# Performance work log

Hardware: AMD Instinct MI355X
Metric: run time of the kernel (lower is better)

The kernel has to match this reference:

```python
import jax, jax.numpy as jnp
import numpy as np

# hardcoded constants from the source module
C = 768      # n_embd
H = 8        # n_head
HS = C // H  # head_size = 96
E = 8        # n_experts
K = 2        # top_k
L = 12       # n_layer
V = 95       # vocab_size = len(chars)
BS = 64      # block_size
B, T = 16, 64


def setup_inputs() -> dict:
    key = jax.random.key(0)
    ks = iter(jax.random.split(key, 32))
    nrm = lambda shape: jax.random.normal(next(ks), shape, dtype=jnp.float32) * 0.02
    d = {
        'idx': jax.random.randint(next(ks), (B, T), 0, V),
        'tok_emb': nrm((V, C)),
        'pos_emb': nrm((BS, C)),
        # attention (per-layer stacked); per-head q/k/v linears concatenated into [C, C]
        'Wq': nrm((L, C, C)), 'Wk': nrm((L, C, C)), 'Wv': nrm((L, C, C)),
        'Wo': nrm((L, C, C)), 'bo': jnp.zeros((L, C), jnp.float32),
        # MoE
        'gate_W': nrm((L, C, E)), 'gate_b': jnp.zeros((L, E), jnp.float32),
        'W1': nrm((L, E, C, 4 * C)), 'b1': jnp.zeros((L, E, 4 * C), jnp.float32),
        'W2': nrm((L, E, 4 * C, C)), 'b2': jnp.zeros((L, E, C), jnp.float32),
        # layernorms
        'ln1_g': jnp.ones((L, C), jnp.float32), 'ln1_b': jnp.zeros((L, C), jnp.float32),
        'ln2_g': jnp.ones((L, C), jnp.float32), 'ln2_b': jnp.zeros((L, C), jnp.float32),
        'lnf_g': jnp.ones((C,), jnp.float32), 'lnf_b': jnp.zeros((C,), jnp.float32),
        # lm head
        'head_W': nrm((C, V)), 'head_b': jnp.zeros((V,), jnp.float32),
    }
    return d


def _layernorm(x, g, b, eps=1e-5):
    mu = x.mean(-1, keepdims=True)
    var = ((x - mu) ** 2).mean(-1, keepdims=True)
    return (x - mu) * jax.lax.rsqrt(var + eps) * g + b


def _moe(x, gw, gb, w1, b1, w2, b2):
    # x: [B,T,C]; compute all experts densely then combine top-k (faithful to source)
    xf = x.reshape(-1, C)                                  # [N,C]
    probs = jax.nn.softmax(xf @ gw + gb, axis=-1)          # [N,E]
    tp, ti = jax.lax.top_k(probs, K)                       # [N,K]
    tp = tp / tp.sum(-1, keepdims=True)
    h = jax.nn.gelu(jnp.einsum('nc,ech->neh', xf, w1) + b1, approximate=False)
    eo = jnp.einsum('neh,ehc->nec', h, w2) + b2            # [N,E,C]
    sel = jnp.take_along_axis(eo, ti[:, :, None], axis=1)  # [N,K,C]
    return (tp[:, :, None] * sel).sum(1).reshape(x.shape)


def _forward(idx, tok_emb, pos_emb, Wq, Wk, Wv, Wo, bo, gate_W, gate_b, W1, b1,
             W2, b2, ln1_g, ln1_b, ln2_g, ln2_b, lnf_g, lnf_b, head_W, head_b):
    Bc, Tc = idx.shape
    x = tok_emb[idx] + pos_emb[jnp.arange(Tc) % BS]        # [B,T,C]
    mask = jnp.tril(jnp.ones((Tc, Tc), bool))

    def block(x, p):
        q = (x @ p['Wq']).reshape(Bc, Tc, H, HS)
        k = (x @ p['Wk']).reshape(Bc, Tc, H, HS)
        v = (x @ p['Wv']).reshape(Bc, Tc, H, HS)
        att = jnp.einsum('bqhd,bkhd->bhqk', q, k) * (HS ** -0.5)
        att = jnp.where(mask, att, -jnp.inf)
        w = jax.nn.softmax(att, axis=-1)
        o = jnp.einsum('bhqk,bkhd->bqhd', w, v).reshape(Bc, Tc, C)
        y = o @ p['Wo'] + p['bo']
        x = _layernorm(x + y, p['g1'], p['b1n'])
        y = _moe(x, p['gw'], p['gb'], p['w1'], p['bb1'], p['w2'], p['bb2'])
        x = _layernorm(x + y, p['g2'], p['b2n'])
        return x, None

    params = {'Wq': Wq, 'Wk': Wk, 'Wv': Wv, 'Wo': Wo, 'bo': bo,
              'gw': gate_W, 'gb': gate_b, 'w1': W1, 'bb1': b1, 'w2': W2, 'bb2': b2,
              'g1': ln1_g, 'b1n': ln1_b, 'g2': ln2_g, 'b2n': ln2_b}
    x, _ = jax.lax.scan(block, x, params)
    x = _layernorm(x, lnf_g, lnf_b)
    return x @ head_W + head_b                              # [B,T,V]


def reference(idx, tok_emb, pos_emb, Wq, Wk, Wv, Wo, bo, gate_W, gate_b, W1, b1,
              W2, b2, ln1_g, ln1_b, ln2_g, ln2_b, lnf_g, lnf_b, head_W, head_b):
    return _forward(idx, tok_emb, pos_emb, Wq, Wk, Wv, Wo, bo, gate_W, gate_b,
                    W1, b1, W2, b2, ln1_g, ln1_b, ln2_g, ln2_b, lnf_g, lnf_b,
                    head_W, head_b)
```

## Files before the change

kernel.cpp:

```cpp
#include <hip/hip_runtime.h>
#include <math.h>

#define C    768
#define HN   8
#define HS   96
#define NE   8
#define NL   12
#define NV   95
#define TT   64
#define NB   16
#define NTOK 1024
#define H4   3072
#define NKR  2048
#define NKRP 2176
#define MC   (NTOK * C)

typedef __attribute__((ext_vector_type(8))) short short8;
typedef __attribute__((ext_vector_type(4))) float floatx4;

union U16x8 { uint4 u; short8 s; };
static __device__ __forceinline__ short8 as_s8(uint4 u) { U16x8 x; x.u = u; return x.s; }
static __device__ __forceinline__ uint4 ror16x4(uint4 q) {
  uint4 r;
  r.x = (q.x >> 16) | (q.x << 16);
  r.y = (q.y >> 16) | (q.y << 16);
  r.z = (q.z >> 16) | (q.z << 16);
  r.w = (q.w >> 16) | (q.w << 16);
  return r;
}

static __device__ __forceinline__ unsigned pack_split(float f) {
  unsigned u = __float_as_uint(f);
  unsigned h = (u + 0x7fffu + ((u >> 16) & 1u)) >> 16;
  float d = f - __uint_as_float(h << 16);
  unsigned v = __float_as_uint(d);
  unsigned l = (v + 0x7fffu + ((v >> 16) & 1u)) >> 16;
  return h | (l << 16);
}
static __device__ __forceinline__ float unpack_split(unsigned w) {
  return __uint_as_float(w << 16) + __uint_as_float(w & 0xffff0000u);
}

static __device__ __forceinline__ void gload_lds16(const unsigned* g, unsigned* l) {
  __builtin_amdgcn_global_load_lds(
      (const __attribute__((address_space(1))) unsigned*)g,
      (__attribute__((address_space(3))) unsigned*)l, 16, 0, 0);
}

__global__ void __launch_bounds__(256) k_prep(const float* __restrict__ src,
    unsigned* __restrict__ dst, int K, int N, long matStride, long dstMatStride) {
  int nt = blockIdx.x, kt = blockIdx.y, mz = blockIdx.z;
  const float* W = src + (size_t)mz * matStride;
  unsigned* out = dst + (size_t)mz * dstMatStride
                + ((size_t)nt * (K >> 5) + kt) * 4096;
  __shared__ float ls[32 * 130];
  int tid = threadIdx.x;
  int n0 = nt * 128, k0 = kt * 32;
  #pragma unroll
  for (int p = 0; p < 16; ++p) {
    int idx = p * 256 + tid;
    int k = idx >> 7, c = idx & 127;
    int n = n0 + c;
    ls[k * 130 + c] = (n < N) ? W[(size_t)(k0 + k) * N + n] : 0.f;
  }
  __syncthreads();
  #pragma unroll
  for (int p = 0; p < 16; ++p) {
    int idx = p * 256 + tid;
    int col = idx >> 5, ks = idx & 31;
    int k = ks ^ ((col & 7) << 2);
    out[idx] = pack_split(ls[k * 130 + col]);
  }
}

template<int OUTMODE>
static __device__ __forceinline__ void gemm_body(
    const unsigned* __restrict__ Ap, const int* __restrict__ perm,
    const unsigned* __restrict__ Wt, const float* __restrict__ bias,
    float* __restrict__ outF, unsigned* __restrict__ outP,
    int row0, int Mend, int col0, int N, int K, int kbeg, int kend)
{
  __shared__ __align__(16) unsigned Bt[2][64 * 32];
  const int tid  = threadIdx.x;
  const int lane = tid & 63, wv = tid >> 6;
  const int l16  = lane & 15, lq = lane >> 4;
  const int sw   = (l16 & 7) << 2;

  int ra0 = row0 + wv * 32 + l16;
  int ra1 = ra0 + 16;
  if (ra0 > Mend - 1) ra0 = Mend - 1;
  if (ra1 > Mend - 1) ra1 = Mend - 1;
  if (perm) { ra0 = perm[ra0]; ra1 = perm[ra1]; }
  const unsigned* A0 = Ap + (size_t)ra0 * K;
  const unsigned* A1 = Ap + (size_t)ra1 * K;

  const unsigned* tsrc = Wt + ((size_t)(col0 >> 7) * (K >> 5) + (kbeg >> 5)) * 4096
                       + ((size_t)((col0 >> 6) & 1)) * 2048;
  auto stageB = [&](int buf, int kt) {
    const unsigned* s = tsrc + (size_t)kt * 4096 + wv * 512 + lane * 4;
    unsigned* d = &Bt[buf][wv * 512 + lane * 4];
    gload_lds16(s, d);
    gload_lds16(s + 256, d + 256);
  };

  uint4 ac0[2], ac1[2];
  auto loadA = [&](int kpos, uint4* d0, uint4* d1) {
    const unsigned* p = A0 + kpos;
    d0[0] = *(const uint4*)(p + lq * 4);
    d0[1] = *(const uint4*)(p + 16 + lq * 4);
    p = A1 + kpos;
    d1[0] = *(const uint4*)(p + lq * 4);
    d1[1] = *(const uint4*)(p + 16 + lq * 4);
  };

  floatx4 acc[2][4];
  #pragma unroll
  for (int h = 0; h < 2; ++h)
    #pragma unroll
    for (int f = 0; f < 4; ++f) acc[h][f] = (floatx4){0, 0, 0, 0};

  const int ns = (kend - kbeg) >> 5;
  stageB(0, 0);
  loadA(kbeg, ac0, ac1);

  for (int s = 0; s < ns; ++s) {
    const int b = s & 1;
    __syncthreads();
    if (s + 1 < ns) stageB(b ^ 1, s + 1);
    const int kn = kbeg + ((s + 1 < ns) ? (s + 1) * 32 : s * 32);
    uint4 na0[2], na1[2];
    loadA(kn, na0, na1);
    const unsigned* bp = Bt[b];
    #pragma unroll
    for (int f = 0; f < 4; ++f) {
      const unsigned* base = bp + (f * 16 + l16) * 32;
      uint4 q0 = *(const uint4*)(base + ((4 * lq) ^ sw));
      uint4 q1 = *(const uint4*)(base + ((16 + 4 * lq) ^ sw));
      short8 b0 = as_s8(q0), b0r = as_s8(ror16x4(q0));
      short8 b1 = as_s8(q1), b1r = as_s8(ror16x4(q1));
      short8 a00 = as_s8(ac0[0]), a01 = as_s8(ac0[1]);
      short8 a10 = as_s8(ac1[0]), a11 = as_s8(ac1[1]);
      acc[0][f] = __builtin_amdgcn_mfma_f32_16x16x32_bf16(a00, b0,  acc[0][f], 0, 0, 0);
      acc[1][f] = __builtin_amdgcn_mfma_f32_16x16x32_bf16(a10, b0,  acc[1][f], 0, 0, 0);
      acc[0][f] = __builtin_amdgcn_mfma_f32_16x16x32_bf16(a00, b0r, acc[0][f], 0, 0, 0);
      acc[1][f] = __builtin_amdgcn_mfma_f32_16x16x32_bf16(a10, b0r, acc[1][f], 0, 0, 0);
      acc[0][f] = __builtin_amdgcn_mfma_f32_16x16x32_bf16(a01, b1,  acc[0][f], 0, 0, 0);
      acc[1][f] = __builtin_amdgcn_mfma_f32_16x16x32_bf16(a11, b1,  acc[1][f], 0, 0, 0);
      acc[0][f] = __builtin_amdgcn_mfma_f32_16x16x32_bf16(a01, b1r, acc[0][f], 0, 0, 0);
      acc[1][f] = __builtin_amdgcn_mfma_f32_16x16x32_bf16(a11, b1r, acc[1][f], 0, 0, 0);
    }
    ac0[0] = na0[0]; ac0[1] = na0[1]; ac1[0] = na1[0]; ac1[1] = na1[1];
  }

  const int rb = row0 + wv * 32 + lq * 4;
  #pragma unroll
  for (int h = 0; h < 2; ++h) {
    #pragma unroll
    for (int f = 0; f < 4; ++f) {
      int cc = col0 + f * 16 + l16;
      if (cc < N) {
        float bb = (OUTMODE == 1) ? bias[cc] : 0.f;
        #pragma unroll
        for (int r = 0; r < 4; ++r) {
          int rr = rb + h * 16 + r;
          if (rr < Mend) {
            float v = acc[h][f][r] + bb;
            if (OUTMODE == 1) {
              v = 0.5f * v * (1.f + erff(v * 0.70710678118654752f));
              outP[(size_t)rr * N + cc] = pack_split(v);
            } else {
              outF[(size_t)rr * N + cc] = v;
            }
          }
        }
      }
    }
  }
}

static __device__ __forceinline__ void expert_range(const int* counts, int e,
                                                    int& off, int& cnt) {
  off = 0; cnt = 0;
  #pragma unroll
  for (int i = 0; i < NE; ++i) {
    int c = counts[i];
    if (i < e) off += c;
    if (i == e) cnt = c;
  }
}

__global__ void __launch_bounds__(256, 2) k_qkv(const unsigned* xp, const unsigned* Wq,
    const unsigned* Wk, const unsigned* Wv, float* qkvp) {
  int z = blockIdx.z, mat = z >> 1, ch = z & 1;
  const unsigned* W = mat == 0 ? Wq : (mat == 1 ? Wk : Wv);
  gemm_body<2>(xp, nullptr, W, nullptr, qkvp + (size_t)z * MC, nullptr,
               blockIdx.y * 128, NTOK, blockIdx.x * 64, C, C, ch * 384, (ch + 1) * 384);
}

__global__ void __launch_bounds__(256, 2) k_wo(const unsigned* op, const unsigned* W,
    float* wop) {
  int ch = blockIdx.z;
  gemm_body<2>(op, nullptr, W, nullptr, wop + (size_t)ch * MC, nullptr,
               blockIdx.y * 128, NTOK, blockIdx.x * 64, C, C, ch * 128, (ch + 1) * 128);
}

__global__ void __launch_bounds__(256, 2) k_w1(const unsigned* xp, const int* perm,
    const unsigned* W1, const float* b1, unsigned* Hgp, const int* counts) {
  int e = blockIdx.z, off, cnt;
  expert_range(counts, e, off, cnt);
  int r0 = blockIdx.y * 128;
  if (r0 >= cnt) return;
  gemm_body<1>(xp, perm, W1 + (size_t)e * C * H4, b1 + (size_t)e * H4, nullptr, Hgp,
               off + r0, off + cnt, blockIdx.x * 64, H4, C, 0, C);
}

__global__ void __launch_bounds__(256, 2) k_w2(const unsigned* Hgp, const unsigned* W2,
    float* Ypart, const int* counts) {
  int z = blockIdx.z, e = z >> 2, ch = z & 3;
  int off, cnt;
  expert_range(counts, e, off, cnt);
  int r0 = blockIdx.y * 128;
  if (r0 >= cnt) return;
  gemm_body<2>(Hgp, nullptr, W2 + (size_t)e * H4 * C, nullptr,
               Ypart + (size_t)ch * NKRP * C, nullptr,
               off + r0, off + cnt, blockIdx.x * 64, C, H4, ch * 768, (ch + 1) * 768);
}

__global__ void __launch_bounds__(256, 2) k_head(const unsigned* xp, const unsigned* W,
    float* hpart) {
  int ch = blockIdx.z;
  gemm_body<2>(xp, nullptr, W, nullptr, hpart + (size_t)ch * NTOK * NV, nullptr,
               blockIdx.y * 128, NTOK, blockIdx.x * 64, NV, C, ch * 64, (ch + 1) * 64);
}

__global__ void k_headsum(const float* hpart, const float* headb, float* out) {
  int n = blockIdx.x, c = threadIdx.x;
  if (c < NV) {
    size_t i = (size_t)n * NV + c;
    float s = headb[c];
    #pragma unroll
    for (int ch = 0; ch < 12; ++ch) s += hpart[i + (size_t)ch * NTOK * NV];
    out[i] = s;
  }
}

__global__ void k_embed(const int* __restrict__ idx, const float* __restrict__ tok,
                        const float* __restrict__ pos, unsigned* __restrict__ xp) {
  int n = blockIdx.x; int t = n & (TT - 1);
  int token = idx[n];
  for (int j = threadIdx.x; j < C; j += 256)
    xp[(size_t)n * C + j] = pack_split(tok[(size_t)token * C + j] + pos[(size_t)t * C + j]);
}

static __device__ __forceinline__ void ln_finish(int tid, float* v, const float* g,
                                                 const float* bb, unsigned* outrow,
                                                 float* sp) {
  int lane = tid & 63, wid = tid >> 6;
  float s = v[0] + v[1] + v[2];
  for (int o = 32; o; o >>= 1) s += __shfl_down(s, o);
  if (!lane) sp[wid] = s;
  __syncthreads();
  float mean = (sp[0] + sp[1] + sp[2] + sp[3]) * (1.f / C);
  __syncthreads();
  float d0 = v[0] - mean, d1 = v[1] - mean, d2 = v[2] - mean;
  float qq = d0 * d0 + d1 * d1 + d2 * d2;
  for (int o = 32; o; o >>= 1) qq += __shfl_down(qq, o);
  if (!lane) sp[wid] = qq;
  __syncthreads();
  float var = (sp[0] + sp[1] + sp[2] + sp[3]) * (1.f / C);
  float rs = rsqrtf(var + 1e-5f);
  #pragma unroll
  for (int i = 0; i < 3; ++i) {
    int c = tid + i * 256;
    v[i] = (v[i] - mean) * rs * g[c] + bb[c];
    outrow[c] = pack_split(v[i]);
  }
}

__global__ void __launch_bounds__(256) k_ln1g(unsigned* __restrict__ xp,
    const float* __restrict__ wop, const float* __restrict__ bo,
    const float* __restrict__ g, const float* __restrict__ bb,
    const float* __restrict__ gW, const float* __restrict__ gb,
    int* __restrict__ ti, float* __restrict__ tp, int* __restrict__ pos,
    int* __restrict__ counts) {
  int n = blockIdx.x; int tid = threadIdx.x;
  __shared__ float sp[4];
  __shared__ float gs[4][NE];
  float v[3];
  #pragma unroll
  for (int i = 0; i < 3; ++i) {
    int c = tid + i * 256;
    size_t gi = (size_t)n * C + c;
    float acc = unpack_split(xp[gi]) + bo[c];
    #pragma unroll
    for (int ch = 0; ch < 6; ++ch) acc += wop[gi + (size_t)ch * MC];
    v[i] = acc;
  }
  ln_finish(tid, v, g, bb, xp + (size_t)n * C, sp);
  float a[NE];
  #pragma unroll
  for (int e = 0; e < NE; ++e) a[e] = 0.f;
  #pragma unroll
  for (int i = 0; i < 3; ++i) {
    int c = tid + i * 256;
    const float* gr = gW + (size_t)c * NE;
    #pragma unroll
    for (int e = 0; e < NE; ++e) a[e] += v[i] * gr[e];
  }
  int lane = tid & 63, wid = tid >> 6;
  #pragma unroll
  for (int e = 0; e < NE; ++e)
    for (int o = 32; o; o >>= 1) a[e] += __shfl_down(a[e], o);
  if (!lane)
    #pragma unroll
    for (int e = 0; e < NE; ++e) gs[wid][e] = a[e];
  __syncthreads();
  if (tid == 0) {
    float p[NE]; float m = -1e30f;
    #pragma unroll
    for (int e = 0; e < NE; ++e) {
      p[e] = gs[0][e] + gs[1][e] + gs[2][e] + gs[3][e] + gb[e];
      m = fmaxf(m, p[e]);
    }
    float den = 0.f;
    #pragma unroll
    for (int e = 0; e < NE; ++e) { p[e] = expf(p[e] - m); den += p[e]; }
    float inv = 1.f / den;
    #pragma unroll
    for (int e = 0; e < NE; ++e) p[e] *= inv;
    int e0 = 0;
    for (int e = 1; e < NE; ++e) if (p[e] > p[e0]) e0 = e;
    int e1 = -1;
    for (int e = 0; e < NE; ++e) if (e != e0 && (e1 < 0 || p[e] > p[e1])) e1 = e;
    float ss = p[e0] + p[e1];
    int p0 = atomicAdd(&counts[e0], 1), p1 = atomicAdd(&counts[e1], 1);
    ti[n * 2] = e0;  ti[n * 2 + 1] = e1;
    pos[n * 2] = p0; pos[n * 2 + 1] = p1;
    tp[n * 2] = p[e0] / ss; tp[n * 2 + 1] = p[e1] / ss;
  }
}

__global__ void k_perm(const int* __restrict__ ti, const int* __restrict__ pos,
                       const int* __restrict__ counts, int* __restrict__ rowOf,
                       int* __restrict__ perm) {
  int a = blockIdx.x * 256 + threadIdx.x;
  if (a >= NKRP) return;
  if (a >= NKR) { perm[a] = 0; return; }
  int e = ti[a];
  int off = 0;
  #pragma unroll
  for (int i = 0; i < NE; ++i) if (i < e) off += counts[i];
  int row = off + pos[a];
  rowOf[a] = row;
  perm[row] = a >> 1;
}

__global__ void __launch_bounds__(256) k_ln_moe(unsigned* __restrict__ xp,
    const float* __restrict__ Ypart, const int* __restrict__ rowOf,
    const int* __restrict__ ti, const float* __restrict__ tp,
    const float* __restrict__ b2, const float* __restrict__ g,
    const float* __restrict__ bb) {
  int n = blockIdx.x; int tid = threadIdx.x;
  __shared__ float sp[4];
  int r0 = rowOf[n * 2], r1 = rowOf[n * 2 + 1];
  int e0 = ti[n * 2], e1 = ti[n * 2 + 1];
  float w0 = tp[n * 2], w1 = tp[n * 2 + 1];
  const float* bz0 = b2 + (size_t)e0 * C;
  const float* bz1 = b2 + (size_t)e1 * C;
  float v[3];
  #pragma unroll
  for (int i = 0; i < 3; ++i) {
    int c = tid + i * 256;
    float y0 = bz0[c], y1 = bz1[c];
    #pragma unroll
    for (int ch = 0; ch < 4; ++ch) {
      const float* pl = Ypart + (size_t)ch * NKRP * C;
      y0 += pl[(size_t)r0 * C + c];
      y1 += pl[(size_t)r1 * C + c];
    }
    v[i] = unpack_split(xp[(size_t)n * C + c]) + w0 * y0 + w1 * y1;
  }
  ln_finish(tid, v, g, bb, xp + (size_t)n * C, sp);
}

__global__ void __launch_bounds__(256) k_lnf(unsigned* __restrict__ xp,
    const float* __restrict__ g, const float* __restrict__ bb) {
  int n = blockIdx.x; int tid = threadIdx.x;
  __shared__ float sp[4];
  float v[3];
  #pragma unroll
  for (int i = 0; i < 3; ++i) v[i] = unpack_split(xp[(size_t)n * C + tid + i * 256]);
  ln_finish(tid, v, g, bb, xp + (size_t)n * C, sp);
}

__global__ void __launch_bounds__(256) k_attn(const float* __restrict__ qkvp,
    unsigned* __restrict__ op, int* __restrict__ counts) {
  int bh = blockIdx.x; int b = bh >> 3, h = bh & 7;
  int tid = threadIdx.x;
  if (bh == 0 && tid < NE) counts[tid] = 0;
  __shared__ float qs[TT][HS];
  __shared__ float kv[TT][HS];
  const float* q0 = qkvp;                  const float* q1 = qkvp + MC;
  const float* k0 = qkvp + 2 * (size_t)MC; const float* k1 = qkvp + 3 * (size_t)MC;
  const float* v0 = qkvp + 4 * (size_t)MC; const float* v1 = qkvp + 5 * (size_t)MC;
  for (int i = tid; i < TT * HS; i += 256) {
    int t = i / HS, d = i % HS;
    size_t gi = (size_t)(b * TT + t) * C + h * HS + d;
    qs[t][d] = q0[gi] + q1[gi];
    kv[t][d] = k0[gi] + k1[gi];
  }
  __syncthreads();
  int r = tid >> 2, g = tid & 3;
  const float scale = 0.10206207261596575f;
  float sreg[16];
  {
    const floatx4* q4 = (const floatx4*)&qs[r][0];
    #pragma unroll
    for (int j = 0; j < 16; ++j) {
      int kk = g * 16 + j;
      float s = -1e30f;
      if (kk <= r) {
        const floatx4* k4 = (const floatx4*)&kv[kk][0];
        float a2 = 0.f;
        #pragma unroll
        for (int d4 = 0; d4 < HS / 4; ++d4) {
          floatx4 a = q4[d4], bbv = k4[d4];
          a2 += a[0]*bbv[0] + a[1]*bbv[1] + a[2]*bbv[2] + a[3]*bbv[3];
        }
        s = a2 * scale;
      }
      sreg[j] = s;
    }
  }
  float m = sreg[0];
  #pragma unroll
  for (int j = 1; j < 16; ++j) m = fmaxf(m, sreg[j]);
  m = fmaxf(m, __shfl_xor(m, 1));
  m = fmaxf(m, __shfl_xor(m, 2));
  float den = 0.f;
  #pragma unroll
  for (int j = 0; j < 16; ++j) { sreg[j] = expf(sreg[j] - m); den += sreg[j]; }
  den += __shfl_xor(den, 1);
  den += __shfl_xor(den, 2);
  float inv = 1.f / den;
  __syncthreads();
  float (*psc)[TT] = (float(*)[TT])&qs[0][0];
  #pragma unroll
  for (int j = 0; j < 16; ++j) psc[r][g * 16 + j] = sreg[j] * inv;
  for (int i = tid; i < TT * HS; i += 256) {
    int t = i / HS, d = i % HS;
    size_t gi = (size_t)(b * TT + t) * C + h * HS + d;
    kv[t][d] = v0[gi] + v1[gi];
  }
  __syncthreads();
  floatx4 accv[6];
  #pragma unroll
  for (int cc = 0; cc < 6; ++cc) accv[cc] = (floatx4){0, 0, 0, 0};
  for (int kk = 0; kk < TT; ++kk) {
    float wgt = psc[r][kk];
    const floatx4* v4 = (const floatx4*)&kv[kk][0];
    #pragma unroll
    for (int cc = 0; cc < 6; ++cc) accv[cc] += wgt * v4[g * 6 + cc];
  }
  unsigned* orow = op + (size_t)(b * TT + r) * C + h * HS + g * 24;
  #pragma unroll
  for (int cc = 0; cc < 6; ++cc)
    #pragma unroll
    for (int mm = 0; mm < 4; ++mm) orow[cc * 4 + mm] = pack_split(accv[cc][mm]);
}

extern "C" void kernel_launch(void* const* d_in, const int* in_sizes, int n_in,
                              void* d_out, int out_size, void* d_ws, size_t ws_size,
                              hipStream_t stream) {
  const int*   idx   = (const int*)d_in[0];
  const float* tok   = (const float*)d_in[1];
  const float* pose  = (const float*)d_in[2];
  const float* Wq    = (const float*)d_in[3];
  const float* Wk    = (const float*)d_in[4];
  const float* Wv    = (const float*)d_in[5];
  const float* Wo    = (const float*)d_in[6];
  const float* bo    = (const float*)d_in[7];
  const float* gW    = (const float*)d_in[8];
  const float* gb    = (const float*)d_in[9];
  const float* W1    = (const float*)d_in[10];
  const float* b1    = (const float*)d_in[11];
  const float* W2    = (const float*)d_in[12];
  const float* b2    = (const float*)d_in[13];
  const float* ln1g  = (const float*)d_in[14];
  const float* ln1b  = (const float*)d_in[15];
  const float* ln2g  = (const float*)d_in[16];
  const float* ln2b  = (const float*)d_in[17];
  const float* lnfg  = (const float*)d_in[18];
  const float* lnfb  = (const float*)d_in[19];
  const float* headW = (const float*)d_in[20];
  const float* headb = (const float*)d_in[21];
  float* out = (float*)d_out;

  if (ws_size < (size_t)2200 * 1024 * 1024) return;
  char* w = (char*)d_ws;
  auto allocU = [&](size_t n) { unsigned* p = (unsigned*)w; w += n * 4; return p; };
  auto allocF = [&](size_t n) { float* p = (float*)w; w += n * 4; return p; };
  unsigned* Wqp = allocU((size_t)NL * C * C);
  unsigned* Wkp = allocU((size_t)NL * C * C);
  unsigned* Wvp = allocU((size_t)NL * C * C);
  unsigned* Wop = allocU((size_t)NL * C * C);
  unsigned* W1p = allocU((size_t)NL * NE * C * H4);
  unsigned* W2p = allocU((size_t)NL * NE * H4 * C);
  unsigned* Whp = allocU((size_t)24 * 4096);
  unsigned* xp    = allocU((size_t)MC);
  unsigned* op    = allocU((size_t)MC);
  float*    qkvp  = allocF((size_t)6 * MC);
  float*    wop   = allocF((size_t)6 * MC);
  unsigned* Hgp   = allocU((size_t)NKRP * H4);
  float*    Ypart = allocF((size_t)4 * NKRP * C);
  float*    hpart = allocF((size_t)12 * NTOK * NV);
  float*    tp    = allocF(NKR);
  int* ti     = (int*)w; w += NKR * 4;
  int* posA   = (int*)w; w += NKR * 4;
  int* rowOf  = (int*)w; w += NKR * 4;
  int* perm   = (int*)w; w += NKRP * 4;
  int* counts = (int*)w; w += NE * 4;

  k_prep<<<dim3(6, 24, 12), 256, 0, stream>>>(Wq, Wqp, C, C, (long)C * C, (long)C * C);
  k_prep<<<dim3(6, 24, 12), 256, 0, stream>>>(Wk, Wkp, C, C, (long)C * C, (long)C * C);
  k_prep<<<dim3(6, 24, 12), 256, 0, stream>>>(Wv, Wvp, C, C, (long)C * C, (long)C * C);
  k_prep<<<dim3(6, 24, 12), 256, 0, stream>>>(Wo, Wop, C, C, (long)C * C, (long)C * C);
  k_prep<<<dim3(24, 24, 96), 256, 0, stream>>>(W1, W1p, C, H4, (long)C * H4, (long)C * H4);
  k_prep<<<dim3(6, 96, 96), 256, 0, stream>>>(W2, W2p, H4, C, (long)H4 * C, (long)H4 * C);
  k_prep<<<dim3(1, 24, 1), 256, 0, stream>>>(headW, Whp, C, NV, 0, 0);

  k_embed<<<NTOK, 256, 0, stream>>>(idx, tok, pose, xp);

  for (int l = 0; l < NL; ++l) {
    k_qkv<<<dim3(12, 8, 6), 256, 0, stream>>>(
        xp, Wqp + (size_t)l * C * C, Wkp + (size_t)l * C * C, Wvp + (size_t)l * C * C, qkvp);
    k_attn<<<NB * HN, 256, 0, stream>>>(qkvp, op, counts);
    k_wo<<<dim3(12, 8, 6), 256, 0, stream>>>(op, Wop + (size_t)l * C * C, wop);
    k_ln1g<<<NTOK, 256, 0, stream>>>(xp, wop, bo + (size_t)l * C,
        ln1g + (size_t)l * C, ln1b + (size_t)l * C,
        gW + (size_t)l * C * NE, gb + (size_t)l * NE, ti, tp, posA, counts);
    k_perm<<<(NKRP + 255) / 256, 256, 0, stream>>>(ti, posA, counts, rowOf, perm);
    k_w1<<<dim3(48, 8, 8), 256, 0, stream>>>(xp, perm,
        W1p + (size_t)l * NE * C * H4, b1 + (size_t)l * NE * H4, Hgp, counts);
    k_w2<<<dim3(12, 8, 32), 256, 0, stream>>>(Hgp,
        W2p + (size_t)l * NE * H4 * C, Ypart, counts);
    k_ln_moe<<<NTOK, 256, 0, stream>>>(xp, Ypart, rowOf, ti, tp,
        b2 + (size_t)l * NE * C, ln2g + (size_t)l * C, ln2b + (size_t)l * C);
  }

  k_lnf<<<NTOK, 256, 0, stream>>>(xp, lnfg, lnfb);
  k_head<<<dim3(2, 8, 12), 256, 0, stream>>>(xp, Whp, hpart);
  k_headsum<<<NTOK, 128, 0, stream>>>(hpart, headb, out);
}
```

Before: 4.105 ms.

## Fuse all per-layer kernels into one persistent kernel with grid barriers

Replaces the dozens of per-layer kernel launches with a single persistent kernel of 512 blocks. Each block loops over the tiles of every stage and stages are separated by a software grid barrier built on a global atomic counter. Split-K factors for Wo and the head are also reduced from 6 and 12 chunks to 2, which shrinks the partial buffers and the reduction work. The aim is to remove launch overhead and inter-kernel gaps, at the cost of spin-barrier latency. The design assumes all 512 blocks are co-resident, and the grid can deadlock if they are not.

New measurement: 12.21 ms. 198% more time.

```diff
diff --git a/kernel.cpp b/kernel.cpp
--- a/kernel.cpp
+++ b/kernel.cpp
@@ -14,6 +14,7 @@
 #define NKR  2048
 #define NKRP 2176
 #define MC   (NTOK * C)
+#define NBLK 512
 
 typedef __attribute__((ext_vector_type(8))) short short8;
 typedef __attribute__((ext_vector_type(4))) float floatx4;
@@ -73,14 +74,24 @@
   }
 }
 
+__global__ void k_embed(const int* __restrict__ idx, const float* __restrict__ tok,
+                        const float* __restrict__ pos, unsigned* __restrict__ xp) {
+  int n = blockIdx.x; int t = n & (TT - 1);
+  int token = idx[n];
+  for (int j = threadIdx.x; j < C; j += 256)
+    xp[(size_t)n * C + j] = pack_split(tok[(size_t)token * C + j] + pos[(size_t)t * C + j]);
+}
+
 template<int OUTMODE>
-static __device__ __forceinline__ void gemm_body(
+static __device__ __forceinline__ void gemm_tile(
+    unsigned* shb,
     const unsigned* __restrict__ Ap, const int* __restrict__ perm,
     const unsigned* __restrict__ Wt, const float* __restrict__ bias,
     float* __restrict__ outF, unsigned* __restrict__ outP,
     int row0, int Mend, int col0, int N, int K, int kbeg, int kend)
 {
-  __shared__ __align__(16) unsigned Bt[2][64 * 32];
+  unsigned* Bt0 = shb;
+  unsigned* Bt1 = shb + 2048;
   const int tid  = threadIdx.x;
   const int lane = tid & 63, wv = tid >> 6;
   const int l16  = lane & 15, lq = lane >> 4;
@@ -98,7 +109,7 @@
                        + ((size_t)((col0 >> 6) & 1)) * 2048;
   auto stageB = [&](int buf, int kt) {
     const unsigned* s = tsrc + (size_t)kt * 4096 + wv * 512 + lane * 4;
-    unsigned* d = &Bt[buf][wv * 512 + lane * 4];
+    unsigned* d = (buf ? Bt1 : Bt0) + wv * 512 + lane * 4;
     gload_lds16(s, d);
     gload_lds16(s + 256, d + 256);
   };
@@ -130,7 +141,7 @@
     const int kn = kbeg + ((s + 1 < ns) ? (s + 1) * 32 : s * 32);
     uint4 na0[2], na1[2];
     loadA(kn, na0, na1);
-    const unsigned* bp = Bt[b];
+    const unsigned* bp = b ? Bt1 : Bt0;
     #pragma unroll
     for (int f = 0; f < 4; ++f) {
       const unsigned* base = bp + (f * 16 + l16) * 32;
@@ -189,72 +200,10 @@
   }
 }
 
-__global__ void __launch_bounds__(256, 2) k_qkv(const unsigned* xp, const unsigned* Wq,
-    const unsigned* Wk, const unsigned* Wv, float* qkvp) {
-  int z = blockIdx.z, mat = z >> 1, ch = z & 1;
-  const unsigned* W = mat == 0 ? Wq : (mat == 1 ? Wk : Wv);
-  gemm_body<2>(xp, nullptr, W, nullptr, qkvp + (size_t)z * MC, nullptr,
-               blockIdx.y * 128, NTOK, blockIdx.x * 64, C, C, ch * 384, (ch + 1) * 384);
-}
-
-__global__ void __launch_bounds__(256, 2) k_wo(const unsigned* op, const unsigned* W,
-    float* wop) {
-  int ch = blockIdx.z;
-  gemm_body<2>(op, nullptr, W, nullptr, wop + (size_t)ch * MC, nullptr,
-               blockIdx.y * 128, NTOK, blockIdx.x * 64, C, C, ch * 128, (ch + 1) * 128);
-}
-
-__global__ void __launch_bounds__(256, 2) k_w1(const unsigned* xp, const int* perm,
-    const unsigned* W1, const float* b1, unsigned* Hgp, const int* counts) {
-  int e = blockIdx.z, off, cnt;
-  expert_range(counts, e, off, cnt);
-  int r0 = blockIdx.y * 128;
-  if (r0 >= cnt) return;
-  gemm_body<1>(xp, perm, W1 + (size_t)e * C * H4, b1 + (size_t)e * H4, nullptr, Hgp,
-               off + r0, off + cnt, blockIdx.x * 64, H4, C, 0, C);
-}
-
-__global__ void __launch_bounds__(256, 2) k_w2(const unsigned* Hgp, const unsigned* W2,
-    float* Ypart, const int* counts) {
-  int z = blockIdx.z, e = z >> 2, ch = z & 3;
-  int off, cnt;
-  expert_range(counts, e, off, cnt);
-  int r0 = blockIdx.y * 128;
-  if (r0 >= cnt) return;
-  gemm_body<2>(Hgp, nullptr, W2 + (size_t)e * H4 * C, nullptr,
-               Ypart + (size_t)ch * NKRP * C, nullptr,
-               off + r0, off + cnt, blockIdx.x * 64, C, H4, ch * 768, (ch + 1) * 768);
-}
-
-__global__ void __launch_bounds__(256, 2) k_head(const unsigned* xp, const unsigned* W,
-    float* hpart) {
-  int ch = blockIdx.z;
-  gemm_body<2>(xp, nullptr, W, nullptr, hpart + (size_t)ch * NTOK * NV, nullptr,
-               blockIdx.y * 128, NTOK, blockIdx.x * 64, NV, C, ch * 64, (ch + 1) * 64);
-}
-
-__global__ void k_headsum(const float* hpart, const float* headb, float* out) {
-  int n = blockIdx.x, c = threadIdx.x;
-  if (c < NV) {
-    size_t i = (size_t)n * NV + c;
-    float s = headb[c];
-    #pragma unroll
-    for (int ch = 0; ch < 12; ++ch) s += hpart[i + (size_t)ch * NTOK * NV];
-    out[i] = s;
-  }
-}
-
-__global__ void k_embed(const int* __restrict__ idx, const float* __restrict__ tok,
-                        const float* __restrict__ pos, unsigned* __restrict__ xp) {
-  int n = blockIdx.x; int t = n & (TT - 1);
-  int token = idx[n];
-  for (int j = threadIdx.x; j < C; j += 256)
-    xp[(size_t)n * C + j] = pack_split(tok[(size_t)token * C + j] + pos[(size_t)t * C + j]);
-}
-
 static __device__ __forceinline__ void ln_finish(int tid, float* v, const float* g,
                                                  const float* bb, unsigned* outrow,
                                                  float* sp) {
+  __syncthreads();
   int lane = tid & 63, wid = tid >> 6;
   float s = v[0] + v[1] + v[2];
   for (int o = 32; o; o >>= 1) s += __shfl_down(s, o);
@@ -277,196 +226,286 @@
   }
 }
 
-__global__ void __launch_bounds__(256) k_ln1g(unsigned* __restrict__ xp,
-    const float* __restrict__ wop, const float* __restrict__ bo,
-    const float* __restrict__ g, const float* __restrict__ bb,
-    const float* __restrict__ gW, const float* __restrict__ gb,
-    int* __restrict__ ti, float* __restrict__ tp, int* __restrict__ pos,
-    int* __restrict__ counts) {
-  int n = blockIdx.x; int tid = threadIdx.x;
-  __shared__ float sp[4];
-  __shared__ float gs[4][NE];
-  float v[3];
-  #pragma unroll
-  for (int i = 0; i < 3; ++i) {
-    int c = tid + i * 256;
-    size_t gi = (size_t)n * C + c;
-    float acc = unpack_split(xp[gi]) + bo[c];
+static __device__ __forceinline__ void gbar(int* bar, int* pc) {
+  __syncthreads();
+  if (threadIdx.x == 0) {
+    __threadfence();
+    atomicAdd(bar, 1);
+    int target = (++(*pc)) * NBLK;
+    while (atomicAdd(bar, 0) < target) __builtin_amdgcn_s_sleep(32);
+  }
+  __syncthreads();
+  __threadfence();
+}
+
+__global__ void __launch_bounds__(256, 2) k_all(
+    const unsigned* Wqp, const unsigned* Wkp, const unsigned* Wvp, const unsigned* Wop,
+    const unsigned* W1p, const unsigned* W2p, const unsigned* Whp,
+    const float* bo, const float* gW, const float* gb,
+    const float* b1, const float* b2,
+    const float* ln1g, const float* ln1b, const float* ln2g, const float* ln2b,
+    const float* lnfg, const float* lnfb, const float* headb,
+    unsigned* xp, unsigned* op, float* qkvp, float* wop,
+    unsigned* Hgp, float* Ypart, float* hpart, float* tp,
+    int* ti, int* posA, int* rowOf, int* perm, int* counts,
+    int* bar, float* out)
+{
+  __shared__ __align__(16) unsigned shb[12288];
+  const int bid = blockIdx.x, tid = threadIdx.x;
+  int pc = 0;
+
+  for (int l = 0; l < NL; ++l) {
+    const unsigned* Wq_l = Wqp + (size_t)l * C * C;
+    const unsigned* Wk_l = Wkp + (size_t)l * C * C;
+    const unsigned* Wv_l = Wvp + (size_t)l * C * C;
+    const unsigned* Wo_l = Wop + (size_t)l * C * C;
+    const unsigned* W1_l = W1p + (size_t)l * NE * C * H4;
+    const unsigned* W2_l = W2p + (size_t)l * NE * H4 * C;
+
+    for (int t = bid; t < 576; t += NBLK) {
+      int bx = t % 12, r = t / 12, by = r & 7, bz = r >> 3;
+      int mat = bz >> 1, ch = bz & 1;
+      const unsigned* W = mat == 0 ? Wq_l : (mat == 1 ? Wk_l : Wv_l);
+      gemm_tile<2>(shb, xp, nullptr, W, nullptr, qkvp + (size_t)bz * MC, nullptr,
+                   by * 128, NTOK, bx * 64, C, C, ch * 384, (ch + 1) * 384);
+    }
+    gbar(bar, &pc);
+
+    if (bid == 0 && tid < NE) counts[tid] = 0;
+    for (int t = bid; t < NB * HN; t += NBLK) {
+      int b = t >> 3, h = t & 7;
+      float (*qs)[HS] = (float(*)[HS])shb;
+      float (*kv)[HS] = (float(*)[HS])(shb + 6144);
+      const float* q0 = qkvp;                  const float* q1 = qkvp + MC;
+      const float* k0 = qkvp + 2 * (size_t)MC; const float* k1 = qkvp + 3 * (size_t)MC;
+      const float* v0 = qkvp + 4 * (size_t)MC; const float* v1 = qkvp + 5 * (size_t)MC;
+      for (int i = tid; i < TT * HS; i += 256) {
+        int tt = i / HS, d = i % HS;
+        size_t gi = (size_t)(b * TT + tt) * C + h * HS + d;
+        qs[tt][d] = q0[gi] + q1[gi];
+        kv[tt][d] = k0[gi] + k1[gi];
+      }
+      __syncthreads();
+      int rr = tid >> 2, g = tid & 3;
+      const float scale = 0.10206207261596575f;
+      float sreg[16];
+      {
+        const floatx4* q4 = (const floatx4*)&qs[rr][0];
+        #pragma unroll
+        for (int j = 0; j < 16; ++j) {
+          int kk = g * 16 + j;
+          float sv = -1e30f;
+          if (kk <= rr) {
+            const floatx4* k4 = (const floatx4*)&kv[kk][0];
+            float a2 = 0.f;
+            #pragma unroll
+            for (int d4 = 0; d4 < HS / 4; ++d4) {
+              floatx4 a = q4[d4], bbv = k4[d4];
+              a2 += a[0]*bbv[0] + a[1]*bbv[1] + a[2]*bbv[2] + a[3]*bbv[3];
+            }
+            sv = a2 * scale;
+          }
+          sreg[j] = sv;
+        }
+      }
+      float m = sreg[0];
+      #pragma unroll
+      for (int j = 1; j < 16; ++j) m = fmaxf(m, sreg[j]);
+      m = fmaxf(m, __shfl_xor(m, 1));
+      m = fmaxf(m, __shfl_xor(m, 2));
+      float den = 0.f;
+      #pragma unroll
+      for (int j = 0; j < 16; ++j) { sreg[j] = expf(sreg[j] - m); den += sreg[j]; }
+      den += __shfl_xor(den, 1);
+      den += __shfl_xor(den, 2);
+      float inv = 1.f / den;
+      __syncthreads();
+      float (*psc)[TT] = (float(*)[TT])&qs[0][0];
+      #pragma unroll
+      for (int j = 0; j < 16; ++j) psc[rr][g * 16 + j] = sreg[j] * inv;
+      for (int i = tid; i < TT * HS; i += 256) {
+        int tt = i / HS, d = i % HS;
+        size_t gi = (size_t)(b * TT + tt) * C + h * HS + d;
+        kv[tt][d] = v0[gi] + v1[gi];
+      }
+      __syncthreads();
+      floatx4 accv[6];
+      #pragma unroll
+      for (int cc = 0; cc < 6; ++cc) accv[cc] = (floatx4){0, 0, 0, 0};
+      for (int kk = 0; kk < TT; ++kk) {
+        float wgt = psc[rr][kk];
+        const floatx4* v4 = (const floatx4*)&kv[kk][0];
+        #pragma unroll
+        for (int cc = 0; cc < 6; ++cc) accv[cc] += wgt * v4[g * 6 + cc];
+      }
+      unsigned* orow = op + (size_t)(b * TT + rr) * C + h * HS + g * 24;
+      #pragma unroll
+      for (int cc = 0; cc < 6; ++cc)
+        #pragma unroll
+        for (int mm = 0; mm < 4; ++mm) orow[cc * 4 + mm] = pack_split(accv[cc][mm]);
+      __syncthreads();
+    }
+    gbar(bar, &pc);
+
+    for (int t = bid; t < 192; t += NBLK) {
+      int bx = t % 12, r = t / 12, by = r & 7, ch = r >> 3;
+      gemm_tile<2>(shb, op, nullptr, Wo_l, nullptr, wop + (size_t)ch * MC, nullptr,
+                   by * 128, NTOK, bx * 64, C, C, ch * 384, (ch + 1) * 384);
+    }
+    gbar(bar, &pc);
+
+    for (int n = bid; n < NTOK; n += NBLK) {
+      float* sp = (float*)shb;
+      float* gs = sp + 4;
+      float v[3];
+      #pragma unroll
+      for (int i = 0; i < 3; ++i) {
+        int c = tid + i * 256;
+        size_t gi = (size_t)n * C + c;
+        float acc = unpack_split(xp[gi]) + bo[(size_t)l * C + c]
+                  + wop[gi] + wop[gi + (size_t)MC];
+        v[i] = acc;
+      }
+      ln_finish(tid, v, ln1g + (size_t)l * C, ln1b + (size_t)l * C, xp + (size_t)n * C, sp);
+      float a[NE];
+      #pragma unroll
+      for (int e = 0; e < NE; ++e) a[e] = 0.f;
+      #pragma unroll
+      for (int i = 0; i < 3; ++i) {
+        int c = tid + i * 256;
+        const float* gr = gW + (size_t)l * C * NE + (size_t)c * NE;
+        #pragma unroll
+        for (int e = 0; e < NE; ++e) a[e] += v[i] * gr[e];
+      }
+      int lane = tid & 63, wid = tid >> 6;
+      #pragma unroll
+      for (int e = 0; e < NE; ++e)
+        for (int o = 32; o; o >>= 1) a[e] += __shfl_down(a[e], o);
+      __syncthreads();
+      if (!lane)
+        #pragma unroll
+        for (int e = 0; e < NE; ++e) gs[wid * NE + e] = a[e];
+      __syncthreads();
+      if (tid == 0) {
+        float p[NE]; float m = -1e30f;
+        #pragma unroll
+        for (int e = 0; e < NE; ++e) {
+          p[e] = gs[e] + gs[NE + e] + gs[2 * NE + e] + gs[3 * NE + e]
+               + gb[(size_t)l * NE + e];
+          m = fmaxf(m, p[e]);
+        }
+        float den = 0.f;
+        #pragma unroll
+        for (int e = 0; e < NE; ++e) { p[e] = expf(p[e] - m); den += p[e]; }
+        float inv = 1.f / den;
+        #pragma unroll
+        for (int e = 0; e < NE; ++e) p[e] *= inv;
+        int e0 = 0;
+        for (int e = 1; e < NE; ++e) if (p[e] > p[e0]) e0 = e;
+        int e1 = -1;
+        for (int e = 0; e < NE; ++e) if (e != e0 && (e1 < 0 || p[e] > p[e1])) e1 = e;
+        float ss = p[e0] + p[e1];
+        int p0 = atomicAdd(&counts[e0], 1), p1 = atomicAdd(&counts[e1], 1);
+        ti[n * 2] = e0;  ti[n * 2 + 1] = e1;
+        posA[n * 2] = p0; posA[n * 2 + 1] = p1;
+        tp[n * 2] = p[e0] / ss; tp[n * 2 + 1] = p[e1] / ss;
+      }
+      __syncthreads();
+    }
+    gbar(bar, &pc);
+
+    {
+      int a = bid * 256 + tid;
+      if (a < NKRP) {
+        if (a >= NKR) perm[a] = 0;
+        else {
+          int e = ti[a];
+          int off = 0;
+          #pragma unroll
+          for (int i = 0; i < NE; ++i) if (i < e) off += counts[i];
+          int row = off + posA[a];
+          rowOf[a] = row;
+          perm[row] = a >> 1;
+        }
+      }
+    }
+    gbar(bar, &pc);
+
+    for (int t = bid; t < 6144; t += NBLK) {
+      int bx = t % 48, r = t / 48, by = r & 15, e = r >> 4;
+      int off, cnt;
+      expert_range(counts, e, off, cnt);
+      int r0 = by * 128;
+      if (r0 >= cnt) continue;
+      gemm_tile<1>(shb, xp, perm, W1_l + (size_t)e * C * H4,
+                   b1 + ((size_t)l * NE + e) * H4, nullptr, Hgp,
+                   off + r0, off + cnt, bx * 64, H4, C, 0, C);
+    }
+    gbar(bar, &pc);
+
+    for (int t = bid; t < 6144; t += NBLK) {
+      int bx = t % 12, r = t / 12, by = r & 15, bz = r >> 4;
+      int e = bz >> 2, ch = bz & 3;
+      int off, cnt;
+      expert_range(counts, e, off, cnt);
+      int r0 = by * 128;
+      if (r0 >= cnt) continue;
+      gemm_tile<2>(shb, Hgp, nullptr, W2_l + (size_t)e * H4 * C, nullptr,
+                   Ypart + (size_t)ch * NKRP * C, nullptr,
+                   off + r0, off + cnt, bx * 64, C, H4, ch * 768, (ch + 1) * 768);
+    }
+    gbar(bar, &pc);
+
+    for (int n = bid; n < NTOK; n += NBLK) {
+      float* sp = (float*)shb;
+      int r0 = rowOf[n * 2], r1 = rowOf[n * 2 + 1];
+      int e0 = ti[n * 2], e1 = ti[n * 2 + 1];
+      float w0 = tp[n * 2], w1v = tp[n * 2 + 1];
+      const float* bz0 = b2 + ((size_t)l * NE + e0) * C;
+      const float* bz1 = b2 + ((size_t)l * NE + e1) * C;
+      float v[3];
+      #pragma unroll
+      for (int i = 0; i < 3; ++i) {
+        int c = tid + i * 256;
+        float y0 = bz0[c], y1 = bz1[c];
+        #pragma unroll
+        for (int ch = 0; ch < 4; ++ch) {
+          const float* pl = Ypart + (size_t)ch * NKRP * C;
+          y0 += pl[(size_t)r0 * C + c];
+          y1 += pl[(size_t)r1 * C + c];
+        }
+        v[i] = unpack_split(xp[(size_t)n * C + c]) + w0 * y0 + w1v * y1;
+      }
+      ln_finish(tid, v, ln2g + (size_t)l * C, ln2b + (size_t)l * C, xp + (size_t)n * C, sp);
+      __syncthreads();
+    }
+    gbar(bar, &pc);
+  }
+
+  for (int n = bid; n < NTOK; n += NBLK) {
+    float* sp = (float*)shb;
+    float v[3];
     #pragma unroll
-    for (int ch = 0; ch < 6; ++ch) acc += wop[gi + (size_t)ch * MC];
-    v[i] = acc;
-  }
-  ln_finish(tid, v, g, bb, xp + (size_t)n * C, sp);
-  float a[NE];
-  #pragma unroll
-  for (int e = 0; e < NE; ++e) a[e] = 0.f;
-  #pragma unroll
-  for (int i = 0; i < 3; ++i) {
-    int c = tid + i * 256;
-    const float* gr = gW + (size_t)c * NE;
-    #pragma unroll
-    for (int e = 0; e < NE; ++e) a[e] += v[i] * gr[e];
-  }
-  int lane = tid & 63, wid = tid >> 6;
-  #pragma unroll
-  for (int e = 0; e < NE; ++e)
-    for (int o = 32; o; o >>= 1) a[e] += __shfl_down(a[e], o);
-  if (!lane)
-    #pragma unroll
-    for (int e = 0; e < NE; ++e) gs[wid][e] = a[e];
-  __syncthreads();
-  if (tid == 0) {
-    float p[NE]; float m = -1e30f;
-    #pragma unroll
-    for (int e = 0; e < NE; ++e) {
-      p[e] = gs[0][e] + gs[1][e] + gs[2][e] + gs[3][e] + gb[e];
-      m = fmaxf(m, p[e]);
-    }
-    float den = 0.f;
-    #pragma unroll
-    for (int e = 0; e < NE; ++e) { p[e] = expf(p[e] - m); den += p[e]; }
-    float inv = 1.f / den;
-    #pragma unroll
-    for (int e = 0; e < NE; ++e) p[e] *= inv;
-    int e0 = 0;
-    for (int e = 1; e < NE; ++e) if (p[e] > p[e0]) e0 = e;
-    int e1 = -1;
-    for (int e = 0; e < NE; ++e) if (e != e0 && (e1 < 0 || p[e] > p[e1])) e1 = e;
-    float ss = p[e0] + p[e1];
-    int p0 = atomicAdd(&counts[e0], 1), p1 = atomicAdd(&counts[e1], 1);
-    ti[n * 2] = e0;  ti[n * 2 + 1] = e1;
-    pos[n * 2] = p0; pos[n * 2 + 1] = p1;
-    tp[n * 2] = p[e0] / ss; tp[n * 2 + 1] = p[e1] / ss;
-  }
-}
-
-__global__ void k_perm(const int* __restrict__ ti, const int* __restrict__ pos,
-                       const int* __restrict__ counts, int* __restrict__ rowOf,
-                       int* __restrict__ perm) {
-  int a = blockIdx.x * 256 + threadIdx.x;
-  if (a >= NKRP) return;
-  if (a >= NKR) { perm[a] = 0; return; }
-  int e = ti[a];
-  int off = 0;
-  #pragma unroll
-  for (int i = 0; i < NE; ++i) if (i < e) off += counts[i];
-  int row = off + pos[a];
-  rowOf[a] = row;
-  perm[row] = a >> 1;
-}
-
-__global__ void __launch_bounds__(256) k_ln_moe(unsigned* __restrict__ xp,
-    const float* __restrict__ Ypart, const int* __restrict__ rowOf,
-    const int* __restrict__ ti, const float* __restrict__ tp,
-    const float* __restrict__ b2, const float* __restrict__ g,
-    const float* __restrict__ bb) {
-  int n = blockIdx.x; int tid = threadIdx.x;
-  __shared__ float sp[4];
-  int r0 = rowOf[n * 2], r1 = rowOf[n * 2 + 1];
-  int e0 = ti[n * 2], e1 = ti[n * 2 + 1];
-  float w0 = tp[n * 2], w1 = tp[n * 2 + 1];
-  const float* bz0 = b2 + (size_t)e0 * C;
-  const float* bz1 = b2 + (size_t)e1 * C;
-  float v[3];
-  #pragma unroll
-  for (int i = 0; i < 3; ++i) {
-    int c = tid + i * 256;
-    float y0 = bz0[c], y1 = bz1[c];
-    #pragma unroll
-    for (int ch = 0; ch < 4; ++ch) {
-      const float* pl = Ypart + (size_t)ch * NKRP * C;
-      y0 += pl[(size_t)r0 * C + c];
-      y1 += pl[(size_t)r1 * C + c];
-    }
-    v[i] = unpack_split(xp[(size_t)n * C + c]) + w0 * y0 + w1 * y1;
-  }
-  ln_finish(tid, v, g, bb, xp + (size_t)n * C, sp);
-}
-
-__global__ void __launch_bounds__(256) k_lnf(unsigned* __restrict__ xp,
-    const float* __restrict__ g, const float* __restrict__ bb) {
-  int n = blockIdx.x; int tid = threadIdx.x;
-  __shared__ float sp[4];
-  float v[3];
-  #pragma unroll
-  for (int i = 0; i < 3; ++i) v[i] = unpack_split(xp[(size_t)n * C + tid + i * 256]);
-  ln_finish(tid, v, g, bb, xp + (size_t)n * C, sp);
-}
-
-__global__ void __launch_bounds__(256) k_attn(const float* __restrict__ qkvp,
-    unsigned* __restrict__ op, int* __restrict__ counts) {
-  int bh = blockIdx.x; int b = bh >> 3, h = bh & 7;
-  int tid = threadIdx.x;
-  if (bh == 0 && tid < NE) counts[tid] = 0;
-  __shared__ float qs[TT][HS];
-  __shared__ float kv[TT][HS];
-  const float* q0 = qkvp;                  const float* q1 = qkvp + MC;
-  const float* k0 = qkvp + 2 * (size_t)MC; const float* k1 = qkvp + 3 * (size_t)MC;
-  const float* v0 = qkvp + 4 * (size_t)MC; const float* v1 = qkvp + 5 * (size_t)MC;
-  for (int i = tid; i < TT * HS; i += 256) {
-    int t = i / HS, d = i % HS;
-    size_t gi = (size_t)(b * TT + t) * C + h * HS + d;
-    qs[t][d] = q0[gi] + q1[gi];
-    kv[t][d] = k0[gi] + k1[gi];
-  }
-  __syncthreads();
-  int r = tid >> 2, g = tid & 3;
-  const float scale = 0.10206207261596575f;
-  float sreg[16];
-  {
-    const floatx4* q4 = (const floatx4*)&qs[r][0];
-    #pragma unroll
-    for (int j = 0; j < 16; ++j) {
-      int kk = g * 16 + j;
-      float s = -1e30f;
-      if (kk <= r) {
-        const floatx4* k4 = (const floatx4*)&kv[kk][0];
-        float a2 = 0.f;
-        #pragma unroll
-        for (int d4 = 0; d4 < HS / 4; ++d4) {
-          floatx4 a = q4[d4], bbv = k4[d4];
-          a2 += a[0]*bbv[0] + a[1]*bbv[1] + a[2]*bbv[2] + a[3]*bbv[3];
-        }
-        s = a2 * scale;
-      }
-      sreg[j] = s;
-    }
-  }
-  float m = sreg[0];
-  #pragma unroll
-  for (int j = 1; j < 16; ++j) m = fmaxf(m, sreg[j]);
-  m = fmaxf(m, __shfl_xor(m, 1));
-  m = fmaxf(m, __shfl_xor(m, 2));
-  float den = 0.f;
-  #pragma unroll
-  for (int j = 0; j < 16; ++j) { sreg[j] = expf(sreg[j] - m); den += sreg[j]; }
-  den += __shfl_xor(den, 1);
-  den += __shfl_xor(den, 2);
-  float inv = 1.f / den;
-  __syncthreads();
-  float (*psc)[TT] = (float(*)[TT])&qs[0][0];
-  #pragma unroll
-  for (int j = 0; j < 16; ++j) psc[r][g * 16 + j] = sreg[j] * inv;
-  for (int i = tid; i < TT * HS; i += 256) {
-    int t = i / HS, d = i % HS;
-    size_t gi = (size_t)(b * TT + t) * C + h * HS + d;
-    kv[t][d] = v0[gi] + v1[gi];
-  }
-  __syncthreads();
-  floatx4 accv[6];
-  #pragma unroll
-  for (int cc = 0; cc < 6; ++cc) accv[cc] = (floatx4){0, 0, 0, 0};
-  for (int kk = 0; kk < TT; ++kk) {
-    float wgt = psc[r][kk];
-    const floatx4* v4 = (const floatx4*)&kv[kk][0];
-    #pragma unroll
-    for (int cc = 0; cc < 6; ++cc) accv[cc] += wgt * v4[g * 6 + cc];
-  }
-  unsigned* orow = op + (size_t)(b * TT + r) * C + h * HS + g * 24;
-  #pragma unroll
-  for (int cc = 0; cc < 6; ++cc)
-    #pragma unroll
-    for (int mm = 0; mm < 4; ++mm) orow[cc * 4 + mm] = pack_split(accv[cc][mm]);
+    for (int i = 0; i < 3; ++i) v[i] = unpack_split(xp[(size_t)n * C + tid + i * 256]);
+    ln_finish(tid, v, lnfg, lnfb, xp + (size_t)n * C, sp);
+    __syncthreads();
+  }
+  gbar(bar, &pc);
+
+  for (int t = bid; t < 32; t += NBLK) {
+    int bx = t & 1, r = t >> 1, by = r & 7, ch = r >> 3;
+    gemm_tile<2>(shb, xp, nullptr, Whp, nullptr,
+                 hpart + (size_t)ch * NTOK * NV, nullptr,
+                 by * 128, NTOK, bx * 64, NV, C, ch * 384, (ch + 1) * 384);
+  }
+  gbar(bar, &pc);
+
+  for (int n = bid; n < NTOK; n += NBLK) {
+    if (tid < NV) {
+      size_t i = (size_t)n * NV + tid;
+      out[i] = hpart[i] + hpart[i + (size_t)NTOK * NV] + headb[tid];
+    }
+  }
 }
 
 extern "C" void kernel_launch(void* const* d_in, const int* in_sizes, int n_in,
@@ -510,16 +549,19 @@
   unsigned* xp    = allocU((size_t)MC);
   unsigned* op    = allocU((size_t)MC);
   float*    qkvp  = allocF((size_t)6 * MC);
-  float*    wop   = allocF((size_t)6 * MC);
+  float*    wop   = allocF((size_t)2 * MC);
   unsigned* Hgp   = allocU((size_t)NKRP * H4);
   float*    Ypart = allocF((size_t)4 * NKRP * C);
-  float*    hpart = allocF((size_t)12 * NTOK * NV);
+  float*    hpart = allocF((size_t)2 * NTOK * NV);
   float*    tp    = allocF(NKR);
   int* ti     = (int*)w; w += NKR * 4;
   int* posA   = (int*)w; w += NKR * 4;
   int* rowOf  = (int*)w; w += NKR * 4;
   int* perm   = (int*)w; w += NKRP * 4;
   int* counts = (int*)w; w += NE * 4;
+  int* bar    = (int*)w; w += 4;
+
+  hipMemsetAsync(bar, 0, sizeof(int), stream);
 
   k_prep<<<dim3(6, 24, 12), 256, 0, stream>>>(Wq, Wqp, C, C, (long)C * C, (long)C * C);
   k_prep<<<dim3(6, 24, 12), 256, 0, stream>>>(Wk, Wkp, C, C, (long)C * C, (long)C * C);
@@ -531,24 +573,9 @@
 
   k_embed<<<NTOK, 256, 0, stream>>>(idx, tok, pose, xp);
 
-  for (int l = 0; l < NL; ++l) {
-    k_qkv<<<dim3(12, 8, 6), 256, 0, stream>>>(
-        xp, Wqp + (size_t)l * C * C, Wkp + (size_t)l * C * C, Wvp + (size_t)l * C * C, qkvp);
-    k_attn<<<NB * HN, 256, 0, stream>>>(qkvp, op, counts);
-    k_wo<<<dim3(12, 8, 6), 256, 0, stream>>>(op, Wop + (size_t)l * C * C, wop);
-    k_ln1g<<<NTOK, 256, 0, stream>>>(xp, wop, bo + (size_t)l * C,
-        ln1g + (size_t)l * C, ln1b + (size_t)l * C,
-        gW + (size_t)l * C * NE, gb + (size_t)l * NE, ti, tp, posA, counts);
-    k_perm<<<(NKRP + 255) / 256, 256, 0, stream>>>(ti, posA, counts, rowOf, perm);
-    k_w1<<<dim3(48, 8, 8), 256, 0, stream>>>(xp, perm,
-        W1p + (size_t)l * NE * C * H4, b1 + (size_t)l * NE * H4, Hgp, counts);
-    k_w2<<<dim3(12, 8, 32), 256, 0, stream>>>(Hgp,
-        W2p + (size_t)l * NE * H4 * C, Ypart, counts);
-    k_ln_moe<<<NTOK, 256, 0, stream>>>(xp, Ypart, rowOf, ti, tp,
-        b2 + (size_t)l * NE * C, ln2g + (size_t)l * C, ln2b + (size_t)l * C);
-  }
-
-  k_lnf<<<NTOK, 256, 0, stream>>>(xp, lnfg, lnfb);
-  k_head<<<dim3(2, 8, 12), 256, 0, stream>>>(xp, Whp, hpart);
-  k_headsum<<<NTOK, 128, 0, stream>>>(hpart, headb, out);
-}
+  k_all<<<NBLK, 256, 0, stream>>>(
+      Wqp, Wkp, Wvp, Wop, W1p, W2p, Whp,
+      bo, gW, gb, b1, b2, ln1g, ln1b, ln2g, ln2b, lnfg, lnfb, headb,
+      xp, op, qkvp, wop, Hgp, Ypart, hpart, tp,
+      ti, posA, rowOf, perm, counts, bar, out);
+}
```
